# Performance work log

Hardware: AMD Instinct MI355X
Metric: run time of the kernel (lower is better)

Reference implementation:

```python
import jax, jax.numpy as jnp
import numpy as np

T = 4096
INPUT_SIZE = 64
DIMS = 64          # __init__ forces dimensions = input_size
RESERVOIR = 2048
OUTPUT_SIZE = 1
SPECTRAL_RADIUS = 0.95


def setup_inputs() -> dict:
    key = jax.random.key(0)
    k_x, k_c, k_in, k_res, k_w, k_b = jax.random.split(key, 6)
    X = jax.random.normal(k_x, (T, INPUT_SIZE, 1), dtype=jnp.float32)
    # conversion matrix: random then QR -> orthonormal columns
    C_raw = jax.random.uniform(k_c, (DIMS, INPUT_SIZE), dtype=jnp.float32)
    C, _ = jnp.linalg.qr(C_raw)
    # ESN weights. W_res entries ~ N(0, 1/RESERVOIR): circular-law spectral
    # radius ~= 1, scaled to the target spectral radius.
    W_in = jax.random.uniform(k_in, (RESERVOIR, DIMS), dtype=jnp.float32, minval=-1.0, maxval=1.0)
    W_res = jax.random.normal(k_res, (RESERVOIR, RESERVOIR), dtype=jnp.float32) * (SPECTRAL_RADIUS / np.sqrt(RESERVOIR))
    dense_W = jax.random.normal(k_w, (OUTPUT_SIZE, RESERVOIR + DIMS), dtype=jnp.float32) * 0.02
    dense_b = jnp.zeros((OUTPUT_SIZE,), dtype=jnp.float32)
    return {"X": X, "C": C, "W_in": W_in, "W_res": W_res,
            "dense_W": dense_W, "dense_b": dense_b}


def reference(X, C, W_in, W_res, dense_W, dense_b):
    # project all inputs up front: u_t = C @ x_t   -> (T, DIMS)
    U = jnp.einsum('di,tio->tdo', C, X)[..., 0]
    # sequential reservoir recurrence: h_t = tanh(W_in u_t + W_res h_{t-1})
    def step(h, u):
        h_new = jnp.tanh(W_in @ u + W_res @ h)
        return h_new, h_new
    h0 = jnp.zeros((W_res.shape[0],), dtype=X.dtype)
    _, H = jax.lax.scan(step, h0, U)            # (T, RESERVOIR)
    # ESN forward returns vstack(u, h); dense1 reads its transpose
    feats = jnp.concatenate([U, H], axis=1)     # (T, DIMS + RESERVOIR)
    y = feats @ dense_W.T + dense_b             # (T, OUTPUT_SIZE)
    # torch: stack of (1, OUTPUT) rows -> (T,1,OUT), permute(0,2,1) -> (T,OUT,1)
    return y[:, :, None]
```

## Files before the change

kernel.cpp:

```cpp
#include <hip/hip_runtime.h>

#define TT 4096

typedef __attribute__((ext_vector_type(2))) unsigned int u2v;
typedef __attribute__((ext_vector_type(4))) unsigned int u4v;
typedef __attribute__((ext_vector_type(2))) __fp16 f16x2;
typedef __attribute__((ext_vector_type(2))) _Float16 F16x2;
union HU { unsigned int u; f16x2 hf; F16x2 hF; };


__global__ void esn_prep(const float* __restrict__ C,
                         const float* __restrict__ Win,
                         const float* __restrict__ dW,
                         float* __restrict__ M,
                         float* __restrict__ wtil) {
  __shared__ float s[64];
  const int b = blockIdx.x, i = threadIdx.x;
  if (b < 2048) {
    s[i] = Win[b * 64 + i];
    __syncthreads();
    float acc = 0.f;
#pragma unroll 16
    for (int d = 0; d < 64; ++d) acc += s[d] * C[d * 64 + i];
    M[b * 64 + i] = acc;
  } else {
    s[i] = dW[i];
    __syncthreads();
    float acc = 0.f;
    for (int d = 0; d < 64; ++d) acc += s[d] * C[d * 64 + i];
    wtil[i] = acc;
  }
}

__device__ __forceinline__ float fast_tanh(float x) {
  const float e = __builtin_amdgcn_exp2f(x * 2.8853900817779268f);
  return 1.0f - 2.0f * __builtin_amdgcn_rcpf(e + 1.0f);
}

__device__ __forceinline__ float fdot2f(const HU a, const HU b, float c) {
#if __has_builtin(__builtin_amdgcn_fdot2)
  return __builtin_amdgcn_fdot2(a.hF, b.hF, c, false);
#else
  return c + (float)a.hf.x * (float)b.hf.x + (float)a.hf.y * (float)b.hf.y;
#endif
}

__global__ __launch_bounds__(1024) void esn_recur(
    const float* __restrict__ X, const float* __restrict__ M,
    const float* __restrict__ W, const float* __restrict__ dW,
    unsigned int* __restrict__ hpub, float* __restrict__ yp) {
  extern __shared__ unsigned int smem[];
  unsigned int* w16 = smem;
  unsigned int* shh = smem + 32768;
  unsigned int* pub = smem + 33792;
  float* psm = (float*)(smem + 33808);
  const int tid = threadIdx.x;
  const int lane = tid & 63;
  const int wave = tid >> 6;
  const int b = blockIdx.x;
  const int r0 = b * 32 + wave * 2;
  const float m0 = M[r0 * 64 + lane];
  const float m1 = M[(r0 + 1) * 64 + lane];
  const float dw0 = dW[64 + r0];
  const float dw1 = dW[64 + r0 + 1];
  for (int i = tid; i < 32768; i += 1024) {
    const int r = i >> 10, j = i & 1023;
    const float2 w2 = *(const float2*)(W + (size_t)(b * 32 + r) * 2048 + 2 * j);
    HU hu; hu.hf = __builtin_amdgcn_cvt_pkrtz(w2.x, w2.y);
    w16[i] = hu.u;
  }
  if (tid < 1024) shh[tid] = 0u;
  __syncthreads();

  for (int t = 0; t < TT; ++t) {
    const float xv = X[t * 64 + lane];
    float a0 = m0 * xv, a1 = m1 * xv;
    const unsigned int* wr0 = w16 + ((wave * 2) << 10);
    const unsigned int* wr1 = wr0 + 1024;
#pragma unroll
    for (int j = 0; j < 4; ++j) {
      const int o = 4 * lane + 256 * j;
      const u4v hv = *(const u4v*)(shh + o);
      const u4v wv0 = *(const u4v*)(wr0 + o);
      const u4v wv1 = *(const u4v*)(wr1 + o);
#pragma unroll
      for (int k = 0; k < 4; ++k) {
        HU ha, wa, wb;
        ha.u = hv[k]; wa.u = wv0[k]; wb.u = wv1[k];
        a0 = fdot2f(wa, ha, a0);
        a1 = fdot2f(wb, ha, a1);
      }
    }
#pragma unroll
    for (int off = 32; off; off >>= 1) {
      a0 += __shfl_xor(a0, off, 64);
      a1 += __shfl_xor(a1, off, 64);
    }
    if (lane == 0) {
      const float h0 = fast_tanh(a0);
      const float h1 = fast_tanh(a1);
      HU pk; pk.hf = __builtin_amdgcn_cvt_pkrtz(h0, h1);
      pub[wave] = pk.u;
      psm[wave] = dw0 * h0 + dw1 * h1;
    }
    __syncthreads();
    const unsigned tg = (unsigned)t + 1u;
    if (wave == 0) {
      if (t + 1 < TT) {
        unsigned int* slot = hpub + ((t & 1) << 11);
        if (tid < 16) {
          u2v pv; pv.x = pub[tid]; pv.y = tg;
          asm volatile("global_store_dwordx2 %0, %1, off sc0 sc1"
                       :: "v"(slot + 2 * (16 * b + tid)), "v"(pv) : "memory");
        }
        const unsigned int* b0 = slot + 2 * lane;
        const unsigned int* b1 = b0 + 1024;
        u2v q0, q1, q2, q3, q4, q5, q6, q7, q8, q9, qa, qb, qc, qd, qe, qf;
        for (;;) {
          asm volatile(
              "global_load_dwordx2 %0, %16, off sc0 sc1\n\t"
              "global_load_dwordx2 %1, %16, off offset:512 sc0 sc1\n\t"
              "global_load_dwordx2 %2, %16, off offset:1024 sc0 sc1\n\t"
              "global_load_dwordx2 %3, %16, off offset:1536 sc0 sc1\n\t"
              "global_load_dwordx2 %4, %16, off offset:2048 sc0 sc1\n\t"
              "global_load_dwordx2 %5, %16, off offset:2560 sc0 sc1\n\t"
              "global_load_dwordx2 %6, %16, off offset:3072 sc0 sc1\n\t"
              "global_load_dwordx2 %7, %16, off offset:3584 sc0 sc1\n\t"
              "global_load_dwordx2 %8, %17, off sc0 sc1\n\t"
              "global_load_dwordx2 %9, %17, off offset:512 sc0 sc1\n\t"
              "global_load_dwordx2 %10, %17, off offset:1024 sc0 sc1\n\t"
              "global_load_dwordx2 %11, %17, off offset:1536 sc0 sc1\n\t"
              "global_load_dwordx2 %12, %17, off offset:2048 sc0 sc1\n\t"
              "global_load_dwordx2 %13, %17, off offset:2560 sc0 sc1\n\t"
              "global_load_dwordx2 %14, %17, off offset:3072 sc0 sc1\n\t"
              "global_load_dwordx2 %15, %17, off offset:3584 sc0 sc1\n\t"
              "s_waitcnt vmcnt(0)"
              : "=&v"(q0), "=&v"(q1), "=&v"(q2), "=&v"(q3),
                "=&v"(q4), "=&v"(q5), "=&v"(q6), "=&v"(q7),
                "=&v"(q8), "=&v"(q9), "=&v"(qa), "=&v"(qb),
                "=&v"(qc), "=&v"(qd), "=&v"(qe), "=&v"(qf)
              : "v"(b0), "v"(b1)
              : "memory");
          bool ok = (q0.y == tg) && (q1.y == tg) && (q2.y == tg) &&
                    (q3.y == tg) && (q4.y == tg) && (q5.y == tg) &&
                    (q6.y == tg) && (q7.y == tg) && (q8.y == tg) &&
                    (q9.y == tg) && (qa.y == tg) && (qb.y == tg) &&
                    (qc.y == tg) && (qd.y == tg) && (qe.y == tg) &&
                    (qf.y == tg);
          if (__all(ok)) break;
        }
        shh[lane] = q0.x;          shh[64 + lane] = q1.x;
        shh[128 + lane] = q2.x;    shh[192 + lane] = q3.x;
        shh[256 + lane] = q4.x;    shh[320 + lane] = q5.x;
        shh[384 + lane] = q6.x;    shh[448 + lane] = q7.x;
        shh[512 + lane] = q8.x;    shh[576 + lane] = q9.x;
        shh[640 + lane] = qa.x;    shh[704 + lane] = qb.x;
        shh[768 + lane] = qc.x;    shh[832 + lane] = qd.x;
        shh[896 + lane] = qe.x;    shh[960 + lane] = qf.x;
      }
    } else if (tid == 64) {
      float s = 0.f;
#pragma unroll
      for (int wv = 0; wv < 16; ++wv) s += psm[wv];
      yp[t * 64 + b] = s;
    }
    __syncthreads();
  }
}

__global__ void esn_out(const float* __restrict__ X,
                        const float* __restrict__ wtil,
                        const float* __restrict__ yp,
                        const float* __restrict__ bptr,
                        float* __restrict__ out) {
  const int tid = threadIdx.x;
  const int lane = tid & 63;
  const int wave = tid >> 6;
  const int t = blockIdx.x * 4 + wave;
  float v = wtil[lane] * X[t * 64 + lane] + yp[t * 64 + lane];
#pragma unroll
  for (int off = 32; off; off >>= 1) v += __shfl_xor(v, off, 64);
  if (lane == 0) out[t] = v + bptr[0];
}

#define ESN_LDS_BYTES 135296

struct EsnInit {
  EsnInit() {
    (void)hipFuncSetAttribute(reinterpret_cast<const void*>(&esn_recur),
                              hipFuncAttributeMaxDynamicSharedMemorySize,
                              ESN_LDS_BYTES);
  }
};
static EsnInit g_esn_init;

extern "C" void kernel_launch(void* const* d_in, const int* in_sizes, int n_in,
                              void* d_out, int out_size, void* d_ws, size_t ws_size,
                              hipStream_t stream) {
  const float* X   = (const float*)d_in[0];
  const float* C   = (const float*)d_in[1];
  const float* Win = (const float*)d_in[2];
  const float* W   = (const float*)d_in[3];
  const float* dW  = (const float*)d_in[4];
  const float* db  = (const float*)d_in[5];
  float* ws   = (float*)d_ws;
  float* M    = ws;
  float* wtil = ws + 131072;
  float* yp   = ws + 131200;
  unsigned int* hpub = (unsigned int*)(ws + 393344);

  esn_prep<<<2049, 64, 0, stream>>>(C, Win, dW, M, wtil);

  void* args[] = {(void*)&X, (void*)&M, (void*)&W, (void*)&dW,
                  (void*)&hpub, (void*)&yp};
  (void)hipLaunchCooperativeKernel(reinterpret_cast<void*>(&esn_recur), dim3(64),
                                   dim3(1024), args, ESN_LDS_BYTES, stream);

  esn_out<<<1024, 256, 0, stream>>>(X, wtil, yp, db, (float*)d_out);
}
```

Before: 10.60 ms.

## Publish hidden state per wave and poll in all threads with one barrier

Each wave now writes its packed hidden-state pair and step tag straight to the global exchange buffer, so there is no staging through LDS and no handoff to wave 0. All 1024 threads then poll one exchange entry each, with a short sleep between polls. The LDS hidden-state buffer and the dense-partial buffer are double-buffered and the per-block output sum is deferred by one step. Together this cuts each time step from two block barriers to one. The cost is much more polling traffic across all blocks, plus sleep granularity that can add latency on the critical path.

```diff
diff --git a/kernel.cpp b/kernel.cpp
--- a/kernel.cpp
+++ b/kernel.cpp
@@ -52,8 +52,7 @@
   extern __shared__ unsigned int smem[];
   unsigned int* w16 = smem;
   unsigned int* shh = smem + 32768;
-  unsigned int* pub = smem + 33792;
-  float* psm = (float*)(smem + 33808);
+  float* psm = (float*)(smem + 34816);
   const int tid = threadIdx.x;
   const int lane = tid & 63;
   const int wave = tid >> 6;
@@ -69,18 +68,25 @@
     HU hu; hu.hf = __builtin_amdgcn_cvt_pkrtz(w2.x, w2.y);
     w16[i] = hu.u;
   }
-  if (tid < 1024) shh[tid] = 0u;
+  shh[1024 + tid] = 0u;
   __syncthreads();
 
+  const unsigned int* wr0 = w16 + ((wave * 2) << 10);
+  const unsigned int* wr1 = wr0 + 1024;
   for (int t = 0; t < TT; ++t) {
+    if (tid == 1 && t > 0) {
+      float s = 0.f;
+#pragma unroll
+      for (int wv = 0; wv < 16; ++wv) s += psm[((t - 1) & 1) * 16 + wv];
+      yp[(t - 1) * 64 + b] = s;
+    }
+    const unsigned int* shr = shh + (((t + 1) & 1) << 10);
     const float xv = X[t * 64 + lane];
     float a0 = m0 * xv, a1 = m1 * xv;
-    const unsigned int* wr0 = w16 + ((wave * 2) << 10);
-    const unsigned int* wr1 = wr0 + 1024;
 #pragma unroll
     for (int j = 0; j < 4; ++j) {
       const int o = 4 * lane + 256 * j;
-      const u4v hv = *(const u4v*)(shh + o);
+      const u4v hv = *(const u4v*)(shr + o);
       const u4v wv0 = *(const u4v*)(wr0 + o);
       const u4v wv1 = *(const u4v*)(wr1 + o);
 #pragma unroll
@@ -96,75 +102,38 @@
       a0 += __shfl_xor(a0, off, 64);
       a1 += __shfl_xor(a1, off, 64);
     }
+    const unsigned tg = (unsigned)t + 1u;
+    unsigned int* slot = hpub + ((t & 1) << 11);
     if (lane == 0) {
       const float h0 = fast_tanh(a0);
       const float h1 = fast_tanh(a1);
       HU pk; pk.hf = __builtin_amdgcn_cvt_pkrtz(h0, h1);
-      pub[wave] = pk.u;
-      psm[wave] = dw0 * h0 + dw1 * h1;
+      psm[(t & 1) * 16 + wave] = dw0 * h0 + dw1 * h1;
+      u2v pv; pv.x = pk.u; pv.y = tg;
+      asm volatile("global_store_dwordx2 %0, %1, off sc0 sc1"
+                   :: "v"(slot + 2 * (16 * b + wave)), "v"(pv) : "memory");
+    }
+    if (t + 1 < TT) {
+      const unsigned int* p = slot + 2 * tid;
+      u2v q;
+      asm volatile("global_load_dwordx2 %0, %1, off sc0 sc1\n\t"
+                   "s_waitcnt vmcnt(0)"
+                   : "=&v"(q) : "v"(p) : "memory");
+      while (q.y != tg) {
+        __builtin_amdgcn_s_sleep(1);
+        asm volatile("global_load_dwordx2 %0, %1, off sc0 sc1\n\t"
+                     "s_waitcnt vmcnt(0)"
+                     : "=&v"(q) : "v"(p) : "memory");
+      }
+      shh[((t & 1) << 10) + tid] = q.x;
     }
     __syncthreads();
-    const unsigned tg = (unsigned)t + 1u;
-    if (wave == 0) {
-      if (t + 1 < TT) {
-        unsigned int* slot = hpub + ((t & 1) << 11);
-        if (tid < 16) {
-          u2v pv; pv.x = pub[tid]; pv.y = tg;
-          asm volatile("global_store_dwordx2 %0, %1, off sc0 sc1"
-                       :: "v"(slot + 2 * (16 * b + tid)), "v"(pv) : "memory");
-        }
-        const unsigned int* b0 = slot + 2 * lane;
-        const unsigned int* b1 = b0 + 1024;
-        u2v q0, q1, q2, q3, q4, q5, q6, q7, q8, q9, qa, qb, qc, qd, qe, qf;
-        for (;;) {
-          asm volatile(
-              "global_load_dwordx2 %0, %16, off sc0 sc1\n\t"
-              "global_load_dwordx2 %1, %16, off offset:512 sc0 sc1\n\t"
-              "global_load_dwordx2 %2, %16, off offset:1024 sc0 sc1\n\t"
-              "global_load_dwordx2 %3, %16, off offset:1536 sc0 sc1\n\t"
-              "global_load_dwordx2 %4, %16, off offset:2048 sc0 sc1\n\t"
-              "global_load_dwordx2 %5, %16, off offset:2560 sc0 sc1\n\t"
-              "global_load_dwordx2 %6, %16, off offset:3072 sc0 sc1\n\t"
-              "global_load_dwordx2 %7, %16, off offset:3584 sc0 sc1\n\t"
-              "global_load_dwordx2 %8, %17, off sc0 sc1\n\t"
-              "global_load_dwordx2 %9, %17, off offset:512 sc0 sc1\n\t"
-              "global_load_dwordx2 %10, %17, off offset:1024 sc0 sc1\n\t"
-              "global_load_dwordx2 %11, %17, off offset:1536 sc0 sc1\n\t"
-              "global_load_dwordx2 %12, %17, off offset:2048 sc0 sc1\n\t"
-              "global_load_dwordx2 %13, %17, off offset:2560 sc0 sc1\n\t"
-              "global_load_dwordx2 %14, %17, off offset:3072 sc0 sc1\n\t"
-              "global_load_dwordx2 %15, %17, off offset:3584 sc0 sc1\n\t"
-              "s_waitcnt vmcnt(0)"
-              : "=&v"(q0), "=&v"(q1), "=&v"(q2), "=&v"(q3),
-                "=&v"(q4), "=&v"(q5), "=&v"(q6), "=&v"(q7),
-                "=&v"(q8), "=&v"(q9), "=&v"(qa), "=&v"(qb),
-                "=&v"(qc), "=&v"(qd), "=&v"(qe), "=&v"(qf)
-              : "v"(b0), "v"(b1)
-              : "memory");
-          bool ok = (q0.y == tg) && (q1.y == tg) && (q2.y == tg) &&
-                    (q3.y == tg) && (q4.y == tg) && (q5.y == tg) &&
-                    (q6.y == tg) && (q7.y == tg) && (q8.y == tg) &&
-                    (q9.y == tg) && (qa.y == tg) && (qb.y == tg) &&
-                    (qc.y == tg) && (qd.y == tg) && (qe.y == tg) &&
-                    (qf.y == tg);
-          if (__all(ok)) break;
-        }
-        shh[lane] = q0.x;          shh[64 + lane] = q1.x;
-        shh[128 + lane] = q2.x;    shh[192 + lane] = q3.x;
-        shh[256 + lane] = q4.x;    shh[320 + lane] = q5.x;
-        shh[384 + lane] = q6.x;    shh[448 + lane] = q7.x;
-        shh[512 + lane] = q8.x;    shh[576 + lane] = q9.x;
-        shh[640 + lane] = qa.x;    shh[704 + lane] = qb.x;
-        shh[768 + lane] = qc.x;    shh[832 + lane] = qd.x;
-        shh[896 + lane] = qe.x;    shh[960 + lane] = qf.x;
-      }
-    } else if (tid == 64) {
-      float s = 0.f;
+  }
+  if (tid == 1) {
+    float s = 0.f;
 #pragma unroll
-      for (int wv = 0; wv < 16; ++wv) s += psm[wv];
-      yp[t * 64 + b] = s;
-    }
-    __syncthreads();
+    for (int wv = 0; wv < 16; ++wv) s += psm[((TT - 1) & 1) * 16 + wv];
+    yp[(TT - 1) * 64 + b] = s;
   }
 }
 
@@ -183,7 +152,7 @@
   if (lane == 0) out[t] = v + bptr[0];
 }
 
-#define ESN_LDS_BYTES 135296
+#define ESN_LDS_BYTES 139392
 
 struct EsnInit {
   EsnInit() {
```

After: 14.49 ms. 36.7% more time.
